# Kernel tuning notes

Measured on AMD Instinct MI355X. Metric: run time of the kernel, lower is better.

Reference implementation:

```python
import jax, jax.numpy as jnp
import numpy as np

EMBED, HEADS, LEVELS, POINTS = 256, 8, 3, 4
SPATIAL = np.array([[128, 128], [64, 64], [32, 32]], dtype=np.int64)  # (H, W) per level
B = 2
S = int((SPATIAL[:, 0] * SPATIAL[:, 1]).sum())  # 21504
Q = S  # encoder self-attention: queries == flattened multi-scale features


def grid_sample_bilinear(img, grid):
    """img: [N,C,H,W]; grid: [N,Q,P,2] (x,y) in [-1,1]; bilinear, zeros padding, align_corners=False.
    Returns [N,C,Q,P]."""
    N, C, H, W = img.shape
    _, Qn, Pn, _ = grid.shape
    x = (grid[..., 0] + 1.0) * (W * 0.5) - 0.5
    y = (grid[..., 1] + 1.0) * (H * 0.5) - 0.5
    x0 = jnp.floor(x)
    y0 = jnp.floor(y)
    wx1 = x - x0
    wy1 = y - y0
    x0i = x0.astype(jnp.int32)
    y0i = y0.astype(jnp.int32)
    imgf = img.reshape(N, C, H * W)

    def gather(ix, iy):
        valid = (ix >= 0) & (ix < W) & (iy >= 0) & (iy < H)
        ixc = jnp.clip(ix, 0, W - 1)
        iyc = jnp.clip(iy, 0, H - 1)
        flat = (iyc * W + ixc).reshape(N, -1)  # [N, Q*P]
        v = jax.vmap(lambda im, f: im[:, f])(imgf, flat)  # [N, C, Q*P]
        return jnp.where(valid.reshape(N, 1, -1), v, 0.0)

    w00 = ((1.0 - wx1) * (1.0 - wy1)).reshape(N, 1, -1)
    w01 = (wx1 * (1.0 - wy1)).reshape(N, 1, -1)
    w10 = ((1.0 - wx1) * wy1).reshape(N, 1, -1)
    w11 = (wx1 * wy1).reshape(N, 1, -1)
    out = (gather(x0i, y0i) * w00 + gather(x0i + 1, y0i) * w01
           + gather(x0i, y0i + 1) * w10 + gather(x0i + 1, y0i + 1) * w11)
    return out.reshape(N, C, Qn, Pn)


def msda_forward(hidden_states, encoder_hidden_states, reference_points, shapes_np,
                 sampling_offsets_w, sampling_offsets_b, attention_weights_w, attention_weights_b,
                 value_proj_w, value_proj_b, output_proj_w, output_proj_b):
    Bn, Qn, E = hidden_states.shape
    H, L, P = HEADS, LEVELS, POINTS
    D = E // H
    Sn = encoder_hidden_states.shape[1]
    value = (encoder_hidden_states @ value_proj_w.T + value_proj_b).reshape(Bn, Sn, H, D)
    off = (hidden_states @ sampling_offsets_w.T + sampling_offsets_b).reshape(Bn, Qn, H, L, P, 2)
    aw = hidden_states @ attention_weights_w.T + attention_weights_b
    aw = jax.nn.softmax(aw.reshape(Bn, Qn, H, L * P), axis=-1).reshape(Bn, Qn, H, L, P)
    # offset normalizer is (W, H) per level
    norm = jnp.asarray(np.stack([shapes_np[:, 1], shapes_np[:, 0]], axis=-1), dtype=hidden_states.dtype)
    loc = reference_points[:, :, None, :, None, :] + off / norm[None, None, None, :, None, :]
    grids = 2.0 * loc - 1.0  # [B,Q,H,L,P,2]
    out = jnp.zeros((Bn * H, D, Qn), value.dtype)
    start = 0
    for lvl in range(L):  # small static loop over levels (distinct spatial shapes)
        h, w = int(shapes_np[lvl, 0]), int(shapes_np[lvl, 1])
        val_l = value[:, start:start + h * w].transpose(0, 2, 3, 1).reshape(Bn * H, D, h, w)
        start += h * w
        g = grids[:, :, :, lvl].transpose(0, 2, 1, 3, 4).reshape(Bn * H, Qn, P, 2)
        sampled = grid_sample_bilinear(val_l, g)  # [B*H, D, Q, P]
        w_l = aw[:, :, :, lvl].transpose(0, 2, 1, 3).reshape(Bn * H, 1, Qn, P)
        out = out + (sampled * w_l).sum(-1)
    out = out.reshape(Bn, H * D, Qn).transpose(0, 2, 1)  # [B,Q,E]
    return out @ output_proj_w.T + output_proj_b


def setup_inputs():
    key = jax.random.key(0)
    ks = jax.random.split(key, 11)
    sc = 0.02
    E, H, L, P = EMBED, HEADS, LEVELS, POINTS
    return {
        "hidden_states": jax.random.normal(ks[0], (B, Q, E), jnp.float32),
        "encoder_hidden_states": jax.random.normal(ks[1], (B, S, E), jnp.float32),
        "reference_points": jax.random.uniform(ks[2], (B, Q, L, 2), jnp.float32),
        "spatial_shapes": jnp.asarray(SPATIAL),
        "sampling_offsets_w": jax.random.normal(ks[3], (H * L * P * 2, E), jnp.float32) * sc,
        "sampling_offsets_b": jax.random.normal(ks[4], (H * L * P * 2,), jnp.float32) * sc,
        "attention_weights_w": jax.random.normal(ks[5], (H * L * P, E), jnp.float32) * sc,
        "attention_weights_b": jax.random.normal(ks[6], (H * L * P,), jnp.float32) * sc,
        "value_proj_w": jax.random.normal(ks[7], (E, E), jnp.float32) * sc,
        "value_proj_b": jax.random.normal(ks[8], (E,), jnp.float32) * sc,
        "output_proj_w": jax.random.normal(ks[9], (E, E), jnp.float32) * sc,
        "output_proj_b": jax.random.normal(ks[10], (E,), jnp.float32) * sc,
    }


def reference(hidden_states, encoder_hidden_states, reference_points, spatial_shapes,
              sampling_offsets_w, sampling_offsets_b, attention_weights_w, attention_weights_b,
              value_proj_w, value_proj_b, output_proj_w, output_proj_b):
    shapes_np = np.asarray(spatial_shapes)  # static per-level (H, W)
    return msda_forward(hidden_states, encoder_hidden_states, reference_points, shapes_np,
                        sampling_offsets_w, sampling_offsets_b, attention_weights_w, attention_weights_b,
                        value_proj_w, value_proj_b, output_proj_w, output_proj_b)
```

## Files before the change

### kernel.cpp

```cpp
#include <hip/hip_runtime.h>
#include <hip/hip_bf16.h>

#define EMBED   256
#define HEADS   8
#define LEVELS  3
#define POINTS  4
#define BATCH   2
#define QLEN    21504
#define SLEN    21504
#define MTOT    (BATCH * QLEN)

typedef __attribute__((ext_vector_type(8))) short short8;
typedef __attribute__((ext_vector_type(4))) float f32x4;
typedef __attribute__((ext_vector_type(2))) float f32x2;

__device__ __forceinline__ short f2bf(float x) {
    unsigned u = __builtin_bit_cast(unsigned, x);
    u += 0x7fffu + ((u >> 16) & 1u);
    return (short)(u >> 16);
}
__device__ __forceinline__ f32x2 bfpair(unsigned u) {
    f32x2 r;
    r.x = __builtin_bit_cast(float, u << 16);
    r.y = __builtin_bit_cast(float, u & 0xffff0000u);
    return r;
}
__device__ __forceinline__ void async16(const void* g, void* l) {
    __builtin_amdgcn_global_load_lds((const __attribute__((address_space(1))) void*)g,
                                     (__attribute__((address_space(3))) void*)l, 16, 0, 0);
}

__global__ __launch_bounds__(256)
void pack_weights_kernel(const float* __restrict__ vW, const float* __restrict__ oW,
                         const float* __restrict__ soW, const float* __restrict__ awW,
                         const float* __restrict__ soB, const float* __restrict__ awB,
                         short* __restrict__ vWb, short* __restrict__ oWb,
                         short* __restrict__ soawWb, float* __restrict__ soawB)
{
    int i = blockIdx.x * 256 + threadIdx.x;
    if (i < 65536) {
        vWb[i] = f2bf(vW[i]);
    } else if (i < 131072) {
        int j = i - 65536;
        oWb[j] = f2bf(oW[j]);
    } else if (i < 204800) {
        int j = i - 131072;
        int row = j >> 8, k = j & 255;
        float v = (row < 192) ? soW[row * 256 + k] : awW[(row - 192) * 256 + k];
        soawWb[j] = f2bf(v);
    } else if (i < 205088) {
        int row = i - 204800;
        soawB[row] = (row < 192) ? soB[row] : awB[row - 192];
    }
}

__device__ __forceinline__
void astat_gemm2(const short8 afr[2][8], const short* __restrict__ Wt,
                 const float* __restrict__ bias, int ngroups, int gcols,
                 int rowstrip, short* __restrict__ Ws,
                 int mode, int ldc, void* __restrict__ Cout)
{
    const int tid  = threadIdx.x;
    const int lane = tid & 63;
    const int wv   = tid >> 6;
    const int m16  = lane & 15;
    const int ko   = lane >> 4;
    const int nch  = gcols * 32;
    const int r0   = rowstrip + wv * 32 + ko * 4;

    for (int gidx = 0; gidx < ngroups; ++gidx) {
        const int colbase = gidx * gcols;
        for (int c = tid; c < nch; c += 128) {
            const int colL = c >> 5;
            const int cw   = c & 31;
            const int csw  = (cw & 24) | ((cw ^ colL) & 7);
            async16(Wt + (((size_t)(colbase + colL)) << 8) + csw * 8, Ws + c * 8);
        }
        __syncthreads();
        const short8* Wvp = (const short8*)Ws;
        const int nct = gcols >> 4;
        for (int ct = 0; ct < nct; ++ct) {
            const int colL = ct * 16 + m16;
            f32x4 a0 = (f32x4)0.f;
            f32x4 a1 = (f32x4)0.f;
            #pragma unroll
            for (int kt = 0; kt < 8; ++kt) {
                const int g = kt * 4 + ko;
                const int s = (g & 24) | ((g ^ colL) & 7);
                const short8 bfrag = Wvp[colL * 32 + s];
                a0 = __builtin_amdgcn_mfma_f32_16x16x32_bf16(afr[0][kt], bfrag, a0, 0, 0, 0);
                a1 = __builtin_amdgcn_mfma_f32_16x16x32_bf16(afr[1][kt], bfrag, a1, 0, 0, 0);
            }
            const int col = colbase + colL;
            const float bv = bias[col];
            if (mode == 1) {
                const int hh = col >> 5, ch = col & 31;
                #pragma unroll
                for (int rt = 0; rt < 2; ++rt) {
                    const f32x4 a = rt ? a1 : a0;
                    #pragma unroll
                    for (int r = 0; r < 4; ++r) {
                        const int rg = r0 + rt * 16 + r;
                        const int b  = (rg >= SLEN) ? 1 : 0;
                        const int sx = rg - b * SLEN;
                        ((short*)Cout)[(((size_t)(b * 8 + hh)) * SLEN + sx) * 32 + ch] = f2bf(a[r] + bv);
                    }
                }
            } else {
                #pragma unroll
                for (int rt = 0; rt < 2; ++rt) {
                    const f32x4 a = rt ? a1 : a0;
                    #pragma unroll
                    for (int r = 0; r < 4; ++r)
                        ((float*)Cout)[(size_t)(r0 + rt * 16 + r) * ldc + col] = a[r] + bv;
                }
            }
        }
        __syncthreads();
    }
}

__global__ __launch_bounds__(128, 2)
void proj_gemm_kernel(const float* __restrict__ enc, const short* __restrict__ vWb,
                      const float* __restrict__ vB, short* __restrict__ valb,
                      const float* __restrict__ hs, const short* __restrict__ soawWb,
                      const float* __restrict__ soawB, float* __restrict__ offaw)
{
    __shared__ short Ws[64 * 256];
    const int tid = threadIdx.x;
    const int lane = tid & 63, wv = tid >> 6;
    const int m16 = lane & 15, ko = lane >> 4;
    const int rowstrip = blockIdx.y * 64;
    const bool isVal = (blockIdx.x == 0);
    const float* A = isVal ? enc : hs;

    short8 afr[2][8];
    #pragma unroll
    for (int rt = 0; rt < 2; ++rt) {
        const int row = rowstrip + wv * 32 + rt * 16 + m16;
        const float* Af = A + (size_t)row * 256 + ko * 8;
        #pragma unroll
        for (int kt = 0; kt < 8; ++kt) {
            float4 x = *(const float4*)(Af + kt * 32);
            float4 y = *(const float4*)(Af + kt * 32 + 4);
            short8 t;
            t[0] = f2bf(x.x); t[1] = f2bf(x.y); t[2] = f2bf(x.z); t[3] = f2bf(x.w);
            t[4] = f2bf(y.x); t[5] = f2bf(y.y); t[6] = f2bf(y.z); t[7] = f2bf(y.w);
            afr[rt][kt] = t;
        }
    }

    if (isVal) astat_gemm2(afr, vWb,    vB,    4, 64, rowstrip, Ws, 1, 256, valb);
    else       astat_gemm2(afr, soawWb, soawB, 6, 48, rowstrip, Ws, 0, 288, offaw);
}

__global__ __launch_bounds__(128, 2)
void out_gemm_kernel(const short* __restrict__ A, const short* __restrict__ oWb,
                     const float* __restrict__ oB, float* __restrict__ C)
{
    __shared__ short Ws[64 * 256];
    const int tid = threadIdx.x;
    const int lane = tid & 63, wv = tid >> 6;
    const int m16 = lane & 15, ko = lane >> 4;
    const int rowstrip = blockIdx.x * 64;

    short8 afr[2][8];
    #pragma unroll
    for (int rt = 0; rt < 2; ++rt) {
        const int row = rowstrip + wv * 32 + rt * 16 + m16;
        const short* Ab = A + (size_t)row * 256 + ko * 8;
        #pragma unroll
        for (int kt = 0; kt < 8; ++kt) afr[rt][kt] = *(const short8*)(Ab + kt * 32);
    }

    astat_gemm2(afr, oWb, oB, 4, 64, rowstrip, Ws, 0, 256, C);
}

__global__ __launch_bounds__(256, 8)
void msda_sample_kernel(const short* __restrict__ value,
                        const float* __restrict__ offaw,
                        const float* __restrict__ ref,
                        short* __restrict__ attn)
{
    __shared__ int prep[32 * 76];

    const int tid = threadIdx.x;
    const int g   = tid >> 3;
    const int sub = tid & 7;
    const int t   = sub >> 2;

    const int blk = blockIdx.x;
    const int h   = blk & 7;
    const int j   = blk >> 3;
    const int b   = (j >= 672) ? 1 : 0;
    const int qc  = j - b * 672;
    const int q   = qc * 32 + g;
    const int bq  = b * QLEN + q;

    {
        const float* awp = offaw + (size_t)bq * 288 + 192 + h * 12;
        const float4 wa = *(const float4*)(awp);
        const float4 wb = *(const float4*)(awp + 4);
        const float4 wc = *(const float4*)(awp + 8);
        float w[12] = { wa.x, wa.y, wa.z, wa.w, wb.x, wb.y, wb.z, wb.w,
                        wc.x, wc.y, wc.z, wc.w };
        float mx = w[0];
        #pragma unroll
        for (int i = 1; i < 12; ++i) mx = fmaxf(mx, w[i]);
        float s = 0.f;
        #pragma unroll
        for (int i = 0; i < 12; ++i) s += __expf(w[i] - mx);
        const float inv = 1.f / s;

        const float* offp = offaw + (size_t)bq * 288 + h * 24;
        const float* refp = ref + (size_t)bq * 6;
        const int npts = (sub < 4) ? 2 : 1;
        #pragma unroll
        for (int it = 0; it < 2; ++it) {
            if (it >= npts) break;
            const int p  = sub + it * 8;
            const int l  = p >> 2;
            const int Wl = 128 >> l;
            const int st = (l == 0) ? 0 : (l == 1 ? 16384 : 20480);

            const float2 oxy = *(const float2*)(offp + p * 2);
            const float2 rxy = *(const float2*)(refp + 2 * l);
            const float ox = oxy.x, oy = oxy.y;
            const float rx = rxy.x, ry = rxy.y;
            const float a  = __expf(w[p] - mx) * inv;

            const float x = fmaf(rx, (float)Wl, ox - 0.5f);
            const float y = fmaf(ry, (float)Wl, oy - 0.5f);
            const float x0f = floorf(x), y0f = floorf(y);
            const int   x0  = (int)x0f,  y0  = (int)y0f;
            const float wx1 = x - x0f, wy1 = y - y0f;
            const float wx0 = 1.f - wx1, wy0 = 1.f - wy1;
            const bool vy0 = (unsigned)y0       < (unsigned)Wl;
            const bool vy1 = (unsigned)(y0 + 1) < (unsigned)Wl;

            const int xs = min(max(x0, 0), Wl - 2);
            const float wl0 = (xs == x0) ? wx0 : ((xs == x0 + 1) ? wx1 : 0.f);
            const float wl1 = (xs == x0) ? wx1 : ((xs + 1 == x0) ? wx0 : 0.f);

            const int hb = (b * 8 + h) * SLEN + st;
            const int o0 = vy0 ? (hb + y0 * Wl + xs) * 64       : 0;
            const int o1 = vy1 ? (hb + (y0 + 1) * Wl + xs) * 64 : 0;

            int* pp = &prep[g * 76 + p * 6];
            pp[0] = o0;
            pp[1] = o1;
            pp[2] = __builtin_bit_cast(int, vy0 ? wy0 * wl0 * a : 0.f);
            pp[3] = __builtin_bit_cast(int, vy0 ? wy0 * wl1 * a : 0.f);
            pp[4] = __builtin_bit_cast(int, vy1 ? wy1 * wl0 * a : 0.f);
            pp[5] = __builtin_bit_cast(int, vy1 ? wy1 * wl1 * a : 0.f);
        }
    }
    __syncthreads();

    const char* vbytes = (const char*)value;
    const unsigned subb = (unsigned)sub * 16u;
    f32x2 acc2[4];
    acc2[0] = (f32x2)0.f; acc2[1] = (f32x2)0.f;
    acc2[2] = (f32x2)0.f; acc2[3] = (f32x2)0.f;

    #pragma unroll
    for (int pb = 0; pb < 4; ++pb) {
        int4  v[6];
        float wgt[6];
        #pragma unroll
        for (int i = 0; i < 3; ++i) {
            const int p = pb * 3 + i;
            const int* pp = &prep[g * 76 + p * 6];
            const unsigned o0 = (unsigned)pp[0] + subb;
            const unsigned o1 = (unsigned)pp[1] + subb;
            wgt[2*i]   = __builtin_bit_cast(float, pp[2 + t]);
            wgt[2*i+1] = __builtin_bit_cast(float, pp[4 + t]);
            v[2*i]   = *(const int4*)(vbytes + (size_t)o0);
            v[2*i+1] = *(const int4*)(vbytes + (size_t)o1);
        }
        #pragma unroll
        for (int i = 0; i < 6; ++i) {
            f32x2 w2; w2.x = wgt[i]; w2.y = wgt[i];
            acc2[0] = __builtin_elementwise_fma(w2, bfpair((unsigned)v[i].x), acc2[0]);
            acc2[1] = __builtin_elementwise_fma(w2, bfpair((unsigned)v[i].y), acc2[1]);
            acc2[2] = __builtin_elementwise_fma(w2, bfpair((unsigned)v[i].z), acc2[2]);
            acc2[3] = __builtin_elementwise_fma(w2, bfpair((unsigned)v[i].w), acc2[3]);
        }
    }

    #pragma unroll
    for (int j2 = 0; j2 < 4; ++j2) {
        acc2[j2].x += __shfl_xor(acc2[j2].x, 4);
        acc2[j2].y += __shfl_xor(acc2[j2].y, 4);
    }

    if (sub < 4) {
        int4 o;
        o.x = ((unsigned)(unsigned short)f2bf(acc2[0].y) << 16) | (unsigned short)f2bf(acc2[0].x);
        o.y = ((unsigned)(unsigned short)f2bf(acc2[1].y) << 16) | (unsigned short)f2bf(acc2[1].x);
        o.z = ((unsigned)(unsigned short)f2bf(acc2[2].y) << 16) | (unsigned short)f2bf(acc2[2].x);
        o.w = ((unsigned)(unsigned short)f2bf(acc2[3].y) << 16) | (unsigned short)f2bf(acc2[3].x);
        ((int4*)attn)[(size_t)bq * 32 + h * 4 + sub] = o;
    }
}

extern "C" void kernel_launch(void* const* d_in, const int* in_sizes, int n_in,
                              void* d_out, int out_size, void* d_ws, size_t ws_size,
                              hipStream_t stream) {
    const float* hs  = (const float*)d_in[0];
    const float* enc = (const float*)d_in[1];
    const float* rp  = (const float*)d_in[2];
    const float* soW = (const float*)d_in[4];
    const float* soB = (const float*)d_in[5];
    const float* awW = (const float*)d_in[6];
    const float* awB = (const float*)d_in[7];
    const float* vW  = (const float*)d_in[8];
    const float* vB  = (const float*)d_in[9];
    const float* oW  = (const float*)d_in[10];
    const float* oB  = (const float*)d_in[11];
    float* out = (float*)d_out;

    const int M = MTOT;
    const size_t ME = (size_t)M * 256;

    short* valb   = (short*)d_ws;
    short* attnb  = valb + ME;
    float* offaw  = (float*)(attnb + ME);
    short* vWb    = (short*)(offaw + (size_t)M * 288);
    short* oWb    = vWb + 65536;
    short* soawWb = oWb + 65536;
    float* soawB  = (float*)(soawWb + 73728);

    pack_weights_kernel<<<dim3(802), dim3(256), 0, stream>>>(vW, oW, soW, awW, soB, awB,
                                                             vWb, oWb, soawWb, soawB);
    proj_gemm_kernel<<<dim3(2, M / 64), dim3(128), 0, stream>>>(enc, vWb, vB, valb,
                                                                hs, soawWb, soawB, offaw);
    msda_sample_kernel<<<dim3(M / 4), dim3(256), 0, stream>>>(valb, offaw, rp, attnb);
    out_gemm_kernel<<<dim3(M / 64), dim3(128), 0, stream>>>(attnb, oWb, oB, out);
}
```

Baseline: 243.1 us.

## Retile projection GEMMs into column-sliced blocks with one weight load

The projection and output GEMMs are restructured so each 512-thread block owns a fixed column slice of the weight matrix (128 or 96 columns) and a 256-row strip. The weight slice is loaded into LDS once, overlapped with the activation-fragment load, instead of looping over column groups with repeated loads and barriers. This removes the per-group syncs and the serialised weight reloads and raises parallelism. In exchange, activation rows are now read once per column slice (2 or 3 times) and LDS use per block doubles.

New measurement: 267.2 us. 9.9% more time.

```diff
diff --git a/kernel.cpp b/kernel.cpp
--- a/kernel.cpp
+++ b/kernel.cpp
@@ -54,91 +54,38 @@
     }
 }
 
-__device__ __forceinline__
-void astat_gemm2(const short8 afr[2][8], const short* __restrict__ Wt,
-                 const float* __restrict__ bias, int ngroups, int gcols,
-                 int rowstrip, short* __restrict__ Ws,
-                 int mode, int ldc, void* __restrict__ Cout)
-{
-    const int tid  = threadIdx.x;
-    const int lane = tid & 63;
-    const int wv   = tid >> 6;
-    const int m16  = lane & 15;
-    const int ko   = lane >> 4;
-    const int nch  = gcols * 32;
-    const int r0   = rowstrip + wv * 32 + ko * 4;
-
-    for (int gidx = 0; gidx < ngroups; ++gidx) {
-        const int colbase = gidx * gcols;
-        for (int c = tid; c < nch; c += 128) {
-            const int colL = c >> 5;
-            const int cw   = c & 31;
-            const int csw  = (cw & 24) | ((cw ^ colL) & 7);
-            async16(Wt + (((size_t)(colbase + colL)) << 8) + csw * 8, Ws + c * 8);
-        }
-        __syncthreads();
-        const short8* Wvp = (const short8*)Ws;
-        const int nct = gcols >> 4;
-        for (int ct = 0; ct < nct; ++ct) {
-            const int colL = ct * 16 + m16;
-            f32x4 a0 = (f32x4)0.f;
-            f32x4 a1 = (f32x4)0.f;
-            #pragma unroll
-            for (int kt = 0; kt < 8; ++kt) {
-                const int g = kt * 4 + ko;
-                const int s = (g & 24) | ((g ^ colL) & 7);
-                const short8 bfrag = Wvp[colL * 32 + s];
-                a0 = __builtin_amdgcn_mfma_f32_16x16x32_bf16(afr[0][kt], bfrag, a0, 0, 0, 0);
-                a1 = __builtin_amdgcn_mfma_f32_16x16x32_bf16(afr[1][kt], bfrag, a1, 0, 0, 0);
-            }
-            const int col = colbase + colL;
-            const float bv = bias[col];
-            if (mode == 1) {
-                const int hh = col >> 5, ch = col & 31;
-                #pragma unroll
-                for (int rt = 0; rt < 2; ++rt) {
-                    const f32x4 a = rt ? a1 : a0;
-                    #pragma unroll
-                    for (int r = 0; r < 4; ++r) {
-                        const int rg = r0 + rt * 16 + r;
-                        const int b  = (rg >= SLEN) ? 1 : 0;
-                        const int sx = rg - b * SLEN;
-                        ((short*)Cout)[(((size_t)(b * 8 + hh)) * SLEN + sx) * 32 + ch] = f2bf(a[r] + bv);
-                    }
-                }
-            } else {
-                #pragma unroll
-                for (int rt = 0; rt < 2; ++rt) {
-                    const f32x4 a = rt ? a1 : a0;
-                    #pragma unroll
-                    for (int r = 0; r < 4; ++r)
-                        ((float*)Cout)[(size_t)(r0 + rt * 16 + r) * ldc + col] = a[r] + bv;
-                }
-            }
-        }
-        __syncthreads();
-    }
-}
-
-__global__ __launch_bounds__(128, 2)
+
+__global__ __launch_bounds__(512, 4)
 void proj_gemm_kernel(const float* __restrict__ enc, const short* __restrict__ vWb,
                       const float* __restrict__ vB, short* __restrict__ valb,
                       const float* __restrict__ hs, const short* __restrict__ soawWb,
                       const float* __restrict__ soawB, float* __restrict__ offaw)
 {
-    __shared__ short Ws[64 * 256];
-    const int tid = threadIdx.x;
+    __shared__ short Ws[128 * 256];
+    const int tid  = threadIdx.x;
     const int lane = tid & 63, wv = tid >> 6;
-    const int m16 = lane & 15, ko = lane >> 4;
-    const int rowstrip = blockIdx.y * 64;
-    const bool isVal = (blockIdx.x == 0);
-    const float* A = isVal ? enc : hs;
-
+    const int m16  = lane & 15, ko = lane >> 4;
+    const int bx   = blockIdx.x;
+    const bool isVal   = (bx < 2);
+    const int  colbase = isVal ? bx * 128 : (bx - 2) * 96;
+    const int  gcols   = isVal ? 128 : 96;
+    const short* Wt    = isVal ? vWb : soawWb;
+    const float* A     = isVal ? enc : hs;
+    const float* bias  = isVal ? vB  : soawB;
+
+    const int nch = gcols * 32;
+    for (int c = tid; c < nch; c += 512) {
+        const int colL = c >> 5;
+        const int cw   = c & 31;
+        const int csw  = (cw & 24) | ((cw ^ colL) & 7);
+        async16(Wt + (((size_t)(colbase + colL)) << 8) + csw * 8, Ws + c * 8);
+    }
+
+    const int strip = blockIdx.y * 256 + wv * 32;
     short8 afr[2][8];
     #pragma unroll
     for (int rt = 0; rt < 2; ++rt) {
-        const int row = rowstrip + wv * 32 + rt * 16 + m16;
-        const float* Af = A + (size_t)row * 256 + ko * 8;
+        const float* Af = A + (size_t)(strip + rt * 16 + m16) * 256 + ko * 8;
         #pragma unroll
         for (int kt = 0; kt < 8; ++kt) {
             float4 x = *(const float4*)(Af + kt * 32);
@@ -149,31 +96,101 @@
             afr[rt][kt] = t;
         }
     }
-
-    if (isVal) astat_gemm2(afr, vWb,    vB,    4, 64, rowstrip, Ws, 1, 256, valb);
-    else       astat_gemm2(afr, soawWb, soawB, 6, 48, rowstrip, Ws, 0, 288, offaw);
-}
-
-__global__ __launch_bounds__(128, 2)
+    __syncthreads();
+
+    const short8* Wvp = (const short8*)Ws;
+    const int r0  = strip + ko * 4;
+    const int nct = gcols >> 4;
+    for (int ct = 0; ct < nct; ++ct) {
+        const int colL = ct * 16 + m16;
+        f32x4 a0 = (f32x4)0.f;
+        f32x4 a1 = (f32x4)0.f;
+        #pragma unroll
+        for (int kt = 0; kt < 8; ++kt) {
+            const int g = kt * 4 + ko;
+            const int s = (g & 24) | ((g ^ colL) & 7);
+            const short8 bfrag = Wvp[colL * 32 + s];
+            a0 = __builtin_amdgcn_mfma_f32_16x16x32_bf16(afr[0][kt], bfrag, a0, 0, 0, 0);
+            a1 = __builtin_amdgcn_mfma_f32_16x16x32_bf16(afr[1][kt], bfrag, a1, 0, 0, 0);
+        }
+        const int col = colbase + colL;
+        const float bv = bias[col];
+        if (isVal) {
+            const int hh = col >> 5, ch = col & 31;
+            #pragma unroll
+            for (int rt = 0; rt < 2; ++rt) {
+                const f32x4 a = rt ? a1 : a0;
+                #pragma unroll
+                for (int r = 0; r < 4; ++r) {
+                    const int rg = r0 + rt * 16 + r;
+                    const int b  = (rg >= SLEN) ? 1 : 0;
+                    const int sx = rg - b * SLEN;
+                    valb[(((size_t)(b * 8 + hh)) * SLEN + sx) * 32 + ch] = f2bf(a[r] + bv);
+                }
+            }
+        } else {
+            #pragma unroll
+            for (int rt = 0; rt < 2; ++rt) {
+                const f32x4 a = rt ? a1 : a0;
+                #pragma unroll
+                for (int r = 0; r < 4; ++r)
+                    offaw[(size_t)(r0 + rt * 16 + r) * 288 + col] = a[r] + bv;
+            }
+        }
+    }
+}
+
+__global__ __launch_bounds__(512, 4)
 void out_gemm_kernel(const short* __restrict__ A, const short* __restrict__ oWb,
                      const float* __restrict__ oB, float* __restrict__ C)
 {
-    __shared__ short Ws[64 * 256];
-    const int tid = threadIdx.x;
+    __shared__ short Ws[128 * 256];
+    const int tid  = threadIdx.x;
     const int lane = tid & 63, wv = tid >> 6;
-    const int m16 = lane & 15, ko = lane >> 4;
-    const int rowstrip = blockIdx.x * 64;
-
+    const int m16  = lane & 15, ko = lane >> 4;
+    const int colbase = blockIdx.x * 128;
+
+    for (int c = tid; c < 4096; c += 512) {
+        const int colL = c >> 5;
+        const int cw   = c & 31;
+        const int csw  = (cw & 24) | ((cw ^ colL) & 7);
+        async16(oWb + (((size_t)(colbase + colL)) << 8) + csw * 8, Ws + c * 8);
+    }
+
+    const int strip = blockIdx.y * 256 + wv * 32;
     short8 afr[2][8];
     #pragma unroll
     for (int rt = 0; rt < 2; ++rt) {
-        const int row = rowstrip + wv * 32 + rt * 16 + m16;
-        const short* Ab = A + (size_t)row * 256 + ko * 8;
+        const short* Ab = A + (size_t)(strip + rt * 16 + m16) * 256 + ko * 8;
         #pragma unroll
         for (int kt = 0; kt < 8; ++kt) afr[rt][kt] = *(const short8*)(Ab + kt * 32);
     }
-
-    astat_gemm2(afr, oWb, oB, 4, 64, rowstrip, Ws, 0, 256, C);
+    __syncthreads();
+
+    const short8* Wvp = (const short8*)Ws;
+    const int r0 = strip + ko * 4;
+    for (int ct = 0; ct < 8; ++ct) {
+        const int colL = ct * 16 + m16;
+        f32x4 a0 = (f32x4)0.f;
+        f32x4 a1 = (f32x4)0.f;
+        #pragma unroll
+        for (int kt = 0; kt < 8; ++kt) {
+            const int g = kt * 4 + ko;
+            const int s = (g & 24) | ((g ^ colL) & 7);
+            const short8 bfrag = Wvp[colL * 32 + s];
+            a0 = __builtin_amdgcn_mfma_f32_16x16x32_bf16(afr[0][kt], bfrag, a0, 0, 0, 0);
+            a1 = __builtin_amdgcn_mfma_f32_16x16x32_bf16(afr[1][kt], bfrag, a1, 0, 0, 0);
+        }
+        const int col = colbase + colL;
+        const float bv = oB[col];
+        #pragma unroll
+        for (int rt = 0; rt < 2; ++rt) {
+            const f32x4 a = rt ? a1 : a0;
+            #pragma unroll
+            for (int r = 0; r < 4; ++r)
+                C[(size_t)(r0 + rt * 16 + r) * 256 + col] = a[r] + bv;
+        }
+    }
 }
 
 __global__ __launch_bounds__(256, 8)
@@ -333,8 +350,8 @@
 
     pack_weights_kernel<<<dim3(802), dim3(256), 0, stream>>>(vW, oW, soW, awW, soB, awB,
                                                              vWb, oWb, soawWb, soawB);
-    proj_gemm_kernel<<<dim3(2, M / 64), dim3(128), 0, stream>>>(enc, vWb, vB, valb,
-                                                                hs, soawWb, soawB, offaw);
+    proj_gemm_kernel<<<dim3(5, 168), dim3(512), 0, stream>>>(enc, vWb, vB, valb,
+                                                             hs, soawWb, soawB, offaw);
     msda_sample_kernel<<<dim3(M / 4), dim3(256), 0, stream>>>(valb, offaw, rp, attnb);
-    out_gemm_kernel<<<dim3(M / 64), dim3(128), 0, stream>>>(attnb, oWb, oB, out);
-}
+    out_gemm_kernel<<<dim3(2, 168), dim3(512), 0, stream>>>(attnb, oWb, oB, out);
+}
```
